# Performance work log

Hardware: AMD Instinct MI355X
Metric: run time of the kernel (lower is better)

The kernel has to match this reference:

```python
import jax, jax.numpy as jnp
import numpy as np

S = 4          # num species
E = 8          # ensemble members (num_batched_networks)
N = 50000      # atoms (single conformer)
AEV = 1008     # aev_dim
ALPHA = 0.1    # CELU alpha (torchani default)
DIMS = [AEV, 256, 192, 160, 1]


def setup_inputs() -> dict:
    key = jax.random.key(0)
    ks = jax.random.split(key, 9)
    # species with exactly N/S atoms per element, randomly permuted
    rs = np.random.RandomState(0)
    sp = np.repeat(np.arange(S), N // S)
    rs.shuffle(sp)
    species = jnp.asarray(sp.reshape(1, N), dtype=jnp.int32)
    # static per-species index lists (equal sizes -> stackable), mirrors cached idx_list
    idx = np.stack([np.nonzero(sp == i)[0] for i in range(S)]).astype(np.int32)  # [S, N//S]
    aev = jax.random.normal(ks[0], (1, N, AEV), dtype=jnp.float32)
    inp = {"aev": aev, "species": species, "idx": jnp.asarray(idx)}
    # per-species, per-ensemble-member weights: W [S,E,din,dout], b [S,E,1,dout]
    for li in range(4):
        din, dout = DIMS[li], DIMS[li + 1]
        kw = jax.random.fold_in(ks[1], li)
        kb = jax.random.fold_in(ks[2], li)
        inp[f"W{li+1}"] = jax.random.normal(kw, (S, E, din, dout), dtype=jnp.float32) / np.sqrt(din).astype(np.float32)
        inp[f"b{li+1}"] = jax.random.normal(kb, (S, E, 1, dout), dtype=jnp.float32) * 0.1
    return inp


def reference(aev, W1, b1, W2, b2, W3, b3, W4, b4, species, idx):
    x = aev.reshape(-1, AEV)                       # flatten(0,1): [N, AEV]
    energies = jnp.zeros((x.shape[0],), dtype=x.dtype)
    celu = lambda v: jax.nn.celu(v, alpha=ALPHA)
    for i in range(S):                              # loop over species (small, static)
        xi = x[idx[i]]                              # gather: [n_i, AEV]
        # BmmAtomicNetwork: expand over ensemble dim, baddbmm chain + CELU
        h = celu(jnp.einsum('ni,eio->eno', xi, W1[i]) + b1[i])   # [E, n_i, 256]
        h = celu(jnp.einsum('eni,eio->eno', h, W2[i]) + b2[i])   # [E, n_i, 192]
        h = celu(jnp.einsum('eni,eio->eno', h, W3[i]) + b3[i])   # [E, n_i, 160]
        h = jnp.einsum('eni,eio->eno', h, W4[i]) + b4[i]          # [E, n_i, 1]
        energies = energies.at[idx[i]].set(h.mean(axis=0).reshape(-1))  # scatter
    # forward: squeeze(0) then sum(0, keepdim=True) -> molecular energy [1]
    return jnp.sum(energies, keepdims=True)
```

## Files before the change

kernel.cpp:

```cpp
#include <hip/hip_runtime.h>

#define S_    4
#define E_    8
#define NPS   12500
#define AEVD  1008
#define D1    256
#define D2    192
#define D3    160
#define TM    64
#define NT    ((NPS + TM - 1) / TM)
#define ALPHA 0.1f

#define KB1 32
#define NB1 16
#define KB2 8
#define NB2 12
#define KB3 6
#define NB3 10

typedef __attribute__((ext_vector_type(8))) short short8;
typedef __attribute__((ext_vector_type(4))) float f32x4;

__device__ __forceinline__ ushort f2bf(float f) {
    unsigned u = __float_as_uint(f);
    unsigned r = u + 0x7FFFu + ((u >> 16) & 1u);
    return (ushort)(r >> 16);
}
__device__ __forceinline__ float bf2f(ushort u) {
    return __uint_as_float(((unsigned)u) << 16);
}
__device__ __forceinline__ float celu_f(float v) {
    return v > 0.0f ? v : ALPHA * (__expf(v * (1.0f / ALPHA)) - 1.0f);
}
__device__ __forceinline__ void sync_lds() {
    asm volatile("s_waitcnt lgkmcnt(0)" ::: "memory");
    __builtin_amdgcn_s_barrier();
}

__device__ __forceinline__ void pack_body(const float* __restrict__ W, ushort* __restrict__ out,
                                          int Ksrc, int kbs, int nbs, int Nsrc, int b)
{
    const int kb = b % kbs;
    const int se = b / kbs;
    const int t  = threadIdx.x;
    const int l  = t & 63, q = t >> 6;
    const float* Wse = W + (size_t)se * Ksrc * Nsrc;
    for (int i = 0; i < 4; ++i) {
        int nb = q + i * 4;
        if (nb >= nbs) break;
        int n = nb * 16 + (l & 15);
        ushort v[8];
        #pragma unroll
        for (int j = 0; j < 8; ++j) {
            int k = kb * 32 + ((l >> 4) << 3) + j;
            float x = (k < Ksrc) ? Wse[(size_t)k * Nsrc + n] : 0.0f;
            v[j] = f2bf(x);
        }
        uint4 u;
        u.x = (unsigned)v[0] | ((unsigned)v[1] << 16);
        u.y = (unsigned)v[2] | ((unsigned)v[3] << 16);
        u.z = (unsigned)v[4] | ((unsigned)v[5] << 16);
        u.w = (unsigned)v[6] | ((unsigned)v[7] << 16);
        *(uint4*)(out + ((((size_t)se * kbs + kb) * nbs + nb) * 64 + l) * 8) = u;
    }
}

__global__ void pack_all(const float* __restrict__ W1, const float* __restrict__ W2,
                         const float* __restrict__ W3,
                         ushort* __restrict__ o1, ushort* __restrict__ o2, ushort* __restrict__ o3)
{
    int b = blockIdx.x;
    if (b < S_ * E_ * KB1)                    pack_body(W1, o1, AEVD, KB1, NB1, D1, b);
    else if (b < S_ * E_ * (KB1 + KB2))       pack_body(W2, o2, D1,   KB2, NB2, D2, b - S_ * E_ * KB1);
    else                                      pack_body(W3, o3, D2,   KB3, NB3, D3, b - S_ * E_ * (KB1 + KB2));
}

__global__ __launch_bounds__(256, 2)
void ani_mfma(const float* __restrict__ aev, const int* __restrict__ idx,
              const ushort* __restrict__ W1p, const ushort* __restrict__ W2p,
              const ushort* __restrict__ W3p,
              const float* __restrict__ b1, const float* __restrict__ b2,
              const float* __restrict__ b3,
              const float* __restrict__ W4, const float* __restrict__ b4,
              float* __restrict__ partials)
{
    const int tile = blockIdx.x;
    const int se   = blockIdx.y;
    const int s    = se >> 3;
    const int t    = threadIdx.x;
    const int w    = t >> 6, l = t & 63;
    const int lm   = l & 15, kq = l >> 4;

    __shared__ ushort H1s[TM][D1 + 8];
    __shared__ ushort H2s[TM][D2 + 8];
    __shared__ __align__(16) ushort Ast[2][4][TM][8];

    const int srow = tile * TM + l;
    const int src  = srow < NPS ? srow : NPS - 1;
    const float* arowp = aev + (size_t)idx[s * NPS + src] * AEVD;
    const int wo = w * 8;

    const ushort* w1se = W1p + (size_t)se * (KB1 * NB1 * 512);

    f32x4 acc1[4][4];
    #pragma unroll
    for (int mi = 0; mi < 4; ++mi)
        #pragma unroll
        for (int j = 0; j < 4; ++j) acc1[mi][j] = (f32x4){0.f, 0.f, 0.f, 0.f};

    uint4 B0[4], B1[4];
    float4 na, nbv;

    auto loadB = [&](uint4* Bt, int kb) {
        #pragma unroll
        for (int i = 0; i < 4; ++i)
            Bt[i] = *(const uint4*)(w1se + ((size_t)(kb * NB1 + (w * 4 + i)) * 64 + l) * 8);
    };
    auto stageA = [&](int kbw) {
        short8 v;
        v[0] = (short)f2bf(na.x);  v[1] = (short)f2bf(na.y);
        v[2] = (short)f2bf(na.z);  v[3] = (short)f2bf(na.w);
        v[4] = (short)f2bf(nbv.x); v[5] = (short)f2bf(nbv.y);
        v[6] = (short)f2bf(nbv.z); v[7] = (short)f2bf(nbv.w);
        *(short8*)&Ast[kbw & 1][w][l][0] = v;
        if (kbw + 1 < KB1) {
            int ko = (kbw + 1) * 32 + wo;
            if (ko > AEVD - 8) ko = AEVD - 8;
            na  = *(const float4*)(arowp + ko);
            nbv = *(const float4*)(arowp + ko + 4);
        }
    };
    auto mfma16 = [&](int buf, uint4* Bt) {
        #pragma unroll
        for (int mi = 0; mi < 4; ++mi) {
            short8 af = *(const short8*)&Ast[buf][kq][mi * 16 + lm][0];
            #pragma unroll
            for (int j = 0; j < 4; ++j)
                acc1[mi][j] = __builtin_amdgcn_mfma_f32_16x16x32_bf16(af, *(short8*)&Bt[j], acc1[mi][j], 0, 0, 0);
        }
    };

    {
        float4 ca = *(const float4*)(arowp + wo);
        float4 cb = *(const float4*)(arowp + wo + 4);
        short8 v;
        v[0] = (short)f2bf(ca.x); v[1] = (short)f2bf(ca.y);
        v[2] = (short)f2bf(ca.z); v[3] = (short)f2bf(ca.w);
        v[4] = (short)f2bf(cb.x); v[5] = (short)f2bf(cb.y);
        v[6] = (short)f2bf(cb.z); v[7] = (short)f2bf(cb.w);
        *(short8*)&Ast[0][w][l][0] = v;
        na  = *(const float4*)(arowp + 32 + wo);
        nbv = *(const float4*)(arowp + 32 + wo + 4);
        loadB(B0, 0);
        loadB(B1, 1);
        sync_lds();
    }

    for (int kb = 0; kb < KB1; kb += 2) {
        if (kb + 1 < KB1) stageA(kb + 1);
        mfma16(0, B0);
        if (kb + 2 < KB1) loadB(B0, kb + 2);
        sync_lds();
        if (kb + 2 < KB1) stageA(kb + 2);
        mfma16(1, B1);
        if (kb + 3 < KB1) loadB(B1, kb + 3);
        sync_lds();
    }
    #pragma unroll
    for (int j = 0; j < 4; ++j) {
        int n = (w * 4 + j) * 16 + lm;
        float bias = b1[se * D1 + n];
        #pragma unroll
        for (int mi = 0; mi < 4; ++mi)
            #pragma unroll
            for (int r = 0; r < 4; ++r)
                H1s[mi * 16 + kq * 4 + r][n] = f2bf(celu_f(acc1[mi][j][r] + bias));
    }
    sync_lds();

    const ushort* w2se = W2p + (size_t)se * (KB2 * NB2 * 512);
    f32x4 acc2[4][3];
    #pragma unroll
    for (int mi = 0; mi < 4; ++mi)
        #pragma unroll
        for (int j = 0; j < 3; ++j) acc2[mi][j] = (f32x4){0.f, 0.f, 0.f, 0.f};

    uint4 C0[3], C1[3];
    auto loadC = [&](uint4* Ct, int kb) {
        #pragma unroll
        for (int i = 0; i < 3; ++i)
            Ct[i] = *(const uint4*)(w2se + ((size_t)(kb * NB2 + (w * 3 + i)) * 64 + l) * 8);
    };
    auto mfma12 = [&](int kb, uint4* Ct) {
        #pragma unroll
        for (int mi = 0; mi < 4; ++mi) {
            short8 af = *(const short8*)&H1s[mi * 16 + lm][kb * 32 + kq * 8];
            #pragma unroll
            for (int j = 0; j < 3; ++j)
                acc2[mi][j] = __builtin_amdgcn_mfma_f32_16x16x32_bf16(af, *(short8*)&Ct[j], acc2[mi][j], 0, 0, 0);
        }
    };
    loadC(C0, 0);
    loadC(C1, 1);
    #pragma unroll
    for (int kb = 0; kb < KB2; kb += 2) {
        mfma12(kb, C0);
        if (kb + 2 < KB2) loadC(C0, kb + 2);
        mfma12(kb + 1, C1);
        if (kb + 3 < KB2) loadC(C1, kb + 3);
    }
    #pragma unroll
    for (int j = 0; j < 3; ++j) {
        int n = (w * 3 + j) * 16 + lm;
        float bias = b2[se * D2 + n];
        #pragma unroll
        for (int mi = 0; mi < 4; ++mi)
            #pragma unroll
            for (int r = 0; r < 4; ++r)
                H2s[mi * 16 + kq * 4 + r][n] = f2bf(celu_f(acc2[mi][j][r] + bias));
    }
    sync_lds();

    const ushort* w3se = W3p + (size_t)se * (KB3 * NB3 * 512);
    const int cw = (w < 2) ? 3 : 2;
    const int ow = (w < 2) ? w * 3 : 6 + (w - 2) * 2;
    f32x4 acc3[4][3];
    #pragma unroll
    for (int mi = 0; mi < 4; ++mi)
        #pragma unroll
        for (int j = 0; j < 3; ++j) acc3[mi][j] = (f32x4){0.f, 0.f, 0.f, 0.f};

    uint4 D0[3], D1v[3];
    auto loadD = [&](uint4* Dt, int kb) {
        #pragma unroll
        for (int i = 0; i < 3; ++i)
            if (i < cw)
                Dt[i] = *(const uint4*)(w3se + ((size_t)(kb * NB3 + (ow + i)) * 64 + l) * 8);
    };
    auto mfma10 = [&](int kb, uint4* Dt) {
        #pragma unroll
        for (int mi = 0; mi < 4; ++mi) {
            short8 af = *(const short8*)&H2s[mi * 16 + lm][kb * 32 + kq * 8];
            #pragma unroll
            for (int j = 0; j < 3; ++j)
                if (j < cw)
                    acc3[mi][j] = __builtin_amdgcn_mfma_f32_16x16x32_bf16(af, *(short8*)&Dt[j], acc3[mi][j], 0, 0, 0);
        }
    };
    loadD(D0, 0);
    loadD(D1v, 1);
    #pragma unroll
    for (int kb = 0; kb < KB3; kb += 2) {
        mfma10(kb, D0);
        if (kb + 2 < KB3) loadD(D0, kb + 2);
        mfma10(kb + 1, D1v);
        if (kb + 3 < KB3) loadD(D1v, kb + 3);
    }
    ushort* H3 = &H1s[0][0];
    #pragma unroll
    for (int j = 0; j < 3; ++j) {
        if (j < cw) {
            int n = (ow + j) * 16 + lm;
            float bias = b3[se * D3 + n];
            #pragma unroll
            for (int mi = 0; mi < 4; ++mi)
                #pragma unroll
                for (int r = 0; r < 4; ++r)
                    H3[(mi * 16 + kq * 4 + r) * (D3 + 8) + n] = f2bf(celu_f(acc3[mi][j][r] + bias));
        }
    }
    float* Wf = (float*)&Ast[0][0][0][0];
    if (t < D3) Wf[t] = W4[se * D3 + t];
    sync_lds();

    const int row = t >> 2, seg = t & 3;
    float sum = 0.0f;
    #pragma unroll
    for (int jj = 0; jj < 40; ++jj) {
        int k = seg * 40 + jj;
        sum += bf2f(H3[row * (D3 + 8) + k]) * Wf[k];
    }
    sum += __shfl_xor(sum, 1);
    sum += __shfl_xor(sum, 2);
    float rowval = (tile * TM + row < NPS) ? (sum + b4[se]) : 0.0f;
    float* Rs = Wf + 256;
    if (seg == 0) Rs[row] = rowval;
    __syncthreads();
    if (t == 0) {
        float tot = 0.0f;
        #pragma unroll
        for (int r = 0; r < TM; ++r) tot += Rs[r];
        partials[tile * (S_ * E_) + se] = tot;
    }
}

__global__ void reduce_partials(const float* __restrict__ p, int n, float* __restrict__ out)
{
    float s = 0.0f;
    for (int i = threadIdx.x; i < n; i += 256) s += p[i];
    #pragma unroll
    for (int o = 32; o > 0; o >>= 1) s += __shfl_xor(s, o);
    __shared__ float sm[4];
    if ((threadIdx.x & 63) == 0) sm[threadIdx.x >> 6] = s;
    __syncthreads();
    if (threadIdx.x == 0) out[0] = (sm[0] + sm[1] + sm[2] + sm[3]) * (1.0f / E_);
}

extern "C" void kernel_launch(void* const* d_in, const int* in_sizes, int n_in,
                              void* d_out, int out_size, void* d_ws, size_t ws_size,
                              hipStream_t stream)
{
    const float* aev = (const float*)d_in[0];
    const int*   idx = (const int*)  d_in[2];
    const float* W1  = (const float*)d_in[3];
    const float* b1  = (const float*)d_in[4];
    const float* W2  = (const float*)d_in[5];
    const float* b2  = (const float*)d_in[6];
    const float* W3  = (const float*)d_in[7];
    const float* b3  = (const float*)d_in[8];
    const float* W4  = (const float*)d_in[9];
    const float* b4  = (const float*)d_in[10];
    float* out = (float*)d_out;

    ushort* w1p = (ushort*)d_ws;
    ushort* w2p = w1p + (size_t)S_ * E_ * KB1 * NB1 * 512;
    ushort* w3p = w2p + (size_t)S_ * E_ * KB2 * NB2 * 512;
    float* partials = (float*)(w3p + (size_t)S_ * E_ * KB3 * NB3 * 512);

    pack_all<<<S_ * E_ * (KB1 + KB2 + KB3), 256, 0, stream>>>(W1, W2, W3, w1p, w2p, w3p);

    dim3 grid(NT, S_ * E_);
    ani_mfma<<<grid, 256, 0, stream>>>(aev, idx, w1p, w2p, w3p,
                                       b1, b2, b3, W4, b4, partials);
    reduce_partials<<<1, 256, 0, stream>>>(partials, NT * S_ * E_, out);
}
```

Measured before the change: 807.7 us.

## Restructure layers 2-3 per-wave row ownership, fuse final layer, regroup grid

Layers 2 and 3 are rewritten so each wave owns 16 rows and computes every output column, with weights as the A operand and activations as B. Each wave writes its layer-2 output back into its own rows of the H1 buffer, so the barrier and the separate H2 buffer go away. Layer 3 output is no longer stored: CELU, the W4 dot product and the b4 bias are applied in registers, followed by a wave shuffle reduction. The grid is reordered so the 32 species-ensemble blocks of 8 neighbouring tiles run close together, which should improve L2 reuse of the gathered AEV rows. LDS use drops and launch bounds rise to 3 blocks per CU, at the risk of register pressure from 12 accumulators and 12 preloaded weight fragments.

```diff
diff --git a/kernel.cpp b/kernel.cpp
--- a/kernel.cpp
+++ b/kernel.cpp
@@ -9,6 +9,8 @@
 #define D3    160
 #define TM    64
 #define NT    ((NPS + TM - 1) / TM)
+#define TG    8
+#define NG    ((NT + TG - 1) / TG)
 #define ALPHA 0.1f
 
 #define KB1 32
@@ -25,9 +27,6 @@
     unsigned u = __float_as_uint(f);
     unsigned r = u + 0x7FFFu + ((u >> 16) & 1u);
     return (ushort)(r >> 16);
-}
-__device__ __forceinline__ float bf2f(ushort u) {
-    return __uint_as_float(((unsigned)u) << 16);
 }
 __device__ __forceinline__ float celu_f(float v) {
     return v > 0.0f ? v : ALPHA * (__expf(v * (1.0f / ALPHA)) - 1.0f);
@@ -75,7 +74,7 @@
     else                                      pack_body(W3, o3, D2,   KB3, NB3, D3, b - S_ * E_ * (KB1 + KB2));
 }
 
-__global__ __launch_bounds__(256, 2)
+__global__ __launch_bounds__(256, 3)
 void ani_mfma(const float* __restrict__ aev, const int* __restrict__ idx,
               const ushort* __restrict__ W1p, const ushort* __restrict__ W2p,
               const ushort* __restrict__ W3p,
@@ -84,15 +83,16 @@
               const float* __restrict__ W4, const float* __restrict__ b4,
               float* __restrict__ partials)
 {
-    const int tile = blockIdx.x;
-    const int se   = blockIdx.y;
-    const int s    = se >> 3;
-    const int t    = threadIdx.x;
-    const int w    = t >> 6, l = t & 63;
-    const int lm   = l & 15, kq = l >> 4;
+    const int se   = blockIdx.x & 31;
+    const int ti   = blockIdx.x >> 5;
+    const int tile = blockIdx.y * TG + ti;
+    if (tile >= NT) return;
+    const int s = se >> 3;
+    const int t = threadIdx.x;
+    const int w = t >> 6, l = t & 63;
+    const int lm = l & 15, kq = l >> 4;
 
     __shared__ ushort H1s[TM][D1 + 8];
-    __shared__ ushort H2s[TM][D2 + 8];
     __shared__ __align__(16) ushort Ast[2][4][TM][8];
 
     const int srow = tile * TM + l;
@@ -178,119 +178,104 @@
     }
     sync_lds();
 
+    ushort* hrow = &H1s[w * 16 + lm][0];
+
     const ushort* w2se = W2p + (size_t)se * (KB2 * NB2 * 512);
-    f32x4 acc2[4][3];
-    #pragma unroll
-    for (int mi = 0; mi < 4; ++mi)
-        #pragma unroll
-        for (int j = 0; j < 3; ++j) acc2[mi][j] = (f32x4){0.f, 0.f, 0.f, 0.f};
-
-    uint4 C0[3], C1[3];
-    auto loadC = [&](uint4* Ct, int kb) {
-        #pragma unroll
-        for (int i = 0; i < 3; ++i)
-            Ct[i] = *(const uint4*)(w2se + ((size_t)(kb * NB2 + (w * 3 + i)) * 64 + l) * 8);
-    };
-    auto mfma12 = [&](int kb, uint4* Ct) {
-        #pragma unroll
-        for (int mi = 0; mi < 4; ++mi) {
-            short8 af = *(const short8*)&H1s[mi * 16 + lm][kb * 32 + kq * 8];
-            #pragma unroll
-            for (int j = 0; j < 3; ++j)
-                acc2[mi][j] = __builtin_amdgcn_mfma_f32_16x16x32_bf16(af, *(short8*)&Ct[j], acc2[mi][j], 0, 0, 0);
-        }
-    };
-    loadC(C0, 0);
-    loadC(C1, 1);
-    #pragma unroll
-    for (int kb = 0; kb < KB2; kb += 2) {
-        mfma12(kb, C0);
-        if (kb + 2 < KB2) loadC(C0, kb + 2);
-        mfma12(kb + 1, C1);
-        if (kb + 3 < KB2) loadC(C1, kb + 3);
-    }
-    #pragma unroll
-    for (int j = 0; j < 3; ++j) {
-        int n = (w * 3 + j) * 16 + lm;
-        float bias = b2[se * D2 + n];
-        #pragma unroll
-        for (int mi = 0; mi < 4; ++mi)
-            #pragma unroll
-            for (int r = 0; r < 4; ++r)
-                H2s[mi * 16 + kq * 4 + r][n] = f2bf(celu_f(acc2[mi][j][r] + bias));
-    }
-    sync_lds();
+    f32x4 acc2[NB2];
+    #pragma unroll
+    for (int i = 0; i < NB2; ++i) acc2[i] = (f32x4){0.f, 0.f, 0.f, 0.f};
+
+    #pragma unroll
+    for (int ch = 0; ch < 2; ++ch) {
+        const int mb0 = ch * 6;
+        uint4 A0[6], A1[6];
+        auto AL2 = [&](int kb, int i) {
+            return *(const uint4*)(w2se + ((size_t)(kb * NB2 + (mb0 + i)) * 64 + l) * 8);
+        };
+        #pragma unroll
+        for (int i = 0; i < 6; ++i) A0[i] = AL2(0, i);
+        short8 bf0 = *(const short8*)(hrow + 0 * 32 + kq * 8);
+        #pragma unroll
+        for (int kb = 0; kb < KB2; kb += 2) {
+            short8 bf1 = *(const short8*)(hrow + (kb + 1) * 32 + kq * 8);
+            #pragma unroll
+            for (int i = 0; i < 6; ++i) A1[i] = AL2(kb + 1, i);
+            #pragma unroll
+            for (int i = 0; i < 6; ++i)
+                acc2[mb0 + i] = __builtin_amdgcn_mfma_f32_16x16x32_bf16(*(short8*)&A0[i], bf0, acc2[mb0 + i], 0, 0, 0);
+            if (kb + 2 < KB2) {
+                bf0 = *(const short8*)(hrow + (kb + 2) * 32 + kq * 8);
+                #pragma unroll
+                for (int i = 0; i < 6; ++i) A0[i] = AL2(kb + 2, i);
+            }
+            #pragma unroll
+            for (int i = 0; i < 6; ++i)
+                acc2[mb0 + i] = __builtin_amdgcn_mfma_f32_16x16x32_bf16(*(short8*)&A1[i], bf1, acc2[mb0 + i], 0, 0, 0);
+        }
+    }
+    #pragma unroll
+    for (int mb = 0; mb < NB2; ++mb) {
+        float4 bv = *(const float4*)&b2[se * D2 + mb * 16 + kq * 4];
+        uint2 u;
+        u.x = (unsigned)f2bf(celu_f(acc2[mb][0] + bv.x)) | ((unsigned)f2bf(celu_f(acc2[mb][1] + bv.y)) << 16);
+        u.y = (unsigned)f2bf(celu_f(acc2[mb][2] + bv.z)) | ((unsigned)f2bf(celu_f(acc2[mb][3] + bv.w)) << 16);
+        *(uint2*)(hrow + mb * 16 + kq * 4) = u;
+    }
 
     const ushort* w3se = W3p + (size_t)se * (KB3 * NB3 * 512);
-    const int cw = (w < 2) ? 3 : 2;
-    const int ow = (w < 2) ? w * 3 : 6 + (w - 2) * 2;
-    f32x4 acc3[4][3];
-    #pragma unroll
-    for (int mi = 0; mi < 4; ++mi)
-        #pragma unroll
-        for (int j = 0; j < 3; ++j) acc3[mi][j] = (f32x4){0.f, 0.f, 0.f, 0.f};
-
-    uint4 D0[3], D1v[3];
-    auto loadD = [&](uint4* Dt, int kb) {
-        #pragma unroll
-        for (int i = 0; i < 3; ++i)
-            if (i < cw)
-                Dt[i] = *(const uint4*)(w3se + ((size_t)(kb * NB3 + (ow + i)) * 64 + l) * 8);
-    };
-    auto mfma10 = [&](int kb, uint4* Dt) {
-        #pragma unroll
-        for (int mi = 0; mi < 4; ++mi) {
-            short8 af = *(const short8*)&H2s[mi * 16 + lm][kb * 32 + kq * 8];
-            #pragma unroll
-            for (int j = 0; j < 3; ++j)
-                if (j < cw)
-                    acc3[mi][j] = __builtin_amdgcn_mfma_f32_16x16x32_bf16(af, *(short8*)&Dt[j], acc3[mi][j], 0, 0, 0);
-        }
-    };
-    loadD(D0, 0);
-    loadD(D1v, 1);
-    #pragma unroll
-    for (int kb = 0; kb < KB3; kb += 2) {
-        mfma10(kb, D0);
-        if (kb + 2 < KB3) loadD(D0, kb + 2);
-        mfma10(kb + 1, D1v);
-        if (kb + 3 < KB3) loadD(D1v, kb + 3);
-    }
-    ushort* H3 = &H1s[0][0];
-    #pragma unroll
-    for (int j = 0; j < 3; ++j) {
-        if (j < cw) {
-            int n = (ow + j) * 16 + lm;
-            float bias = b3[se * D3 + n];
-            #pragma unroll
-            for (int mi = 0; mi < 4; ++mi)
+    f32x4 acc3[NB3];
+    #pragma unroll
+    for (int i = 0; i < NB3; ++i) acc3[i] = (f32x4){0.f, 0.f, 0.f, 0.f};
+
+    #pragma unroll
+    for (int ch = 0; ch < 2; ++ch) {
+        const int mb0 = ch * 5;
+        uint4 A0[5], A1[5];
+        auto AL3 = [&](int kb, int i) {
+            return *(const uint4*)(w3se + ((size_t)(kb * NB3 + (mb0 + i)) * 64 + l) * 8);
+        };
+        #pragma unroll
+        for (int i = 0; i < 5; ++i) A0[i] = AL3(0, i);
+        short8 bf0 = *(const short8*)(hrow + 0 * 32 + kq * 8);
+        #pragma unroll
+        for (int kb = 0; kb < KB3; kb += 2) {
+            short8 bf1 = *(const short8*)(hrow + (kb + 1) * 32 + kq * 8);
+            #pragma unroll
+            for (int i = 0; i < 5; ++i) A1[i] = AL3(kb + 1, i);
+            #pragma unroll
+            for (int i = 0; i < 5; ++i)
+                acc3[mb0 + i] = __builtin_amdgcn_mfma_f32_16x16x32_bf16(*(short8*)&A0[i], bf0, acc3[mb0 + i], 0, 0, 0);
+            if (kb + 2 < KB3) {
+                bf0 = *(const short8*)(hrow + (kb + 2) * 32 + kq * 8);
                 #pragma unroll
-                for (int r = 0; r < 4; ++r)
-                    H3[(mi * 16 + kq * 4 + r) * (D3 + 8) + n] = f2bf(celu_f(acc3[mi][j][r] + bias));
-        }
-    }
-    float* Wf = (float*)&Ast[0][0][0][0];
-    if (t < D3) Wf[t] = W4[se * D3 + t];
-    sync_lds();
-
-    const int row = t >> 2, seg = t & 3;
-    float sum = 0.0f;
-    #pragma unroll
-    for (int jj = 0; jj < 40; ++jj) {
-        int k = seg * 40 + jj;
-        sum += bf2f(H3[row * (D3 + 8) + k]) * Wf[k];
-    }
-    sum += __shfl_xor(sum, 1);
-    sum += __shfl_xor(sum, 2);
-    float rowval = (tile * TM + row < NPS) ? (sum + b4[se]) : 0.0f;
-    float* Rs = Wf + 256;
-    if (seg == 0) Rs[row] = rowval;
+                for (int i = 0; i < 5; ++i) A0[i] = AL3(kb + 2, i);
+            }
+            #pragma unroll
+            for (int i = 0; i < 5; ++i)
+                acc3[mb0 + i] = __builtin_amdgcn_mfma_f32_16x16x32_bf16(*(short8*)&A1[i], bf1, acc3[mb0 + i], 0, 0, 0);
+        }
+    }
+
+    float e = 0.0f;
+    #pragma unroll
+    for (int mb = 0; mb < NB3; ++mb) {
+        float4 b3v = *(const float4*)&b3[se * D3 + mb * 16 + kq * 4];
+        float4 w4v = *(const float4*)&W4[se * D3 + mb * 16 + kq * 4];
+        e += celu_f(acc3[mb][0] + b3v.x) * w4v.x;
+        e += celu_f(acc3[mb][1] + b3v.y) * w4v.y;
+        e += celu_f(acc3[mb][2] + b3v.z) * w4v.z;
+        e += celu_f(acc3[mb][3] + b3v.w) * w4v.w;
+    }
+    if (tile * TM + w * 16 + lm >= NPS) e = 0.0f;
+    #pragma unroll
+    for (int o = 32; o > 0; o >>= 1) e += __shfl_xor(e, o);
+
+    float* red = (float*)&Ast[0][0][0][0];
+    if (l == 0) red[w] = e;
     __syncthreads();
     if (t == 0) {
-        float tot = 0.0f;
-        #pragma unroll
-        for (int r = 0; r < TM; ++r) tot += Rs[r];
-        partials[tile * (S_ * E_) + se] = tot;
+        int nv = NPS - tile * TM; if (nv > TM) nv = TM;
+        partials[tile * (S_ * E_) + se] = red[0] + red[1] + red[2] + red[3] + (float)nv * b4[se];
     }
 }
 
@@ -329,7 +314,7 @@
 
     pack_all<<<S_ * E_ * (KB1 + KB2 + KB3), 256, 0, stream>>>(W1, W2, W3, w1p, w2p, w3p);
 
-    dim3 grid(NT, S_ * E_);
+    dim3 grid(32 * TG, NG);
     ani_mfma<<<grid, 256, 0, stream>>>(aev, idx, w1p, w2p, w3p,
                                        b1, b2, b3, W4, b4, partials);
     reduce_partials<<<1, 256, 0, stream>>>(partials, NT * S_ * E_, out);
```

Result: faster. 790.1 us (-2.2%).
